# Optimization experiments

Hardware: AMD Instinct MI355X
Metric: run time of the kernel (lower is better)

The kernel has to match this reference:

```python
import jax, jax.numpy as jnp
import numpy as np
from jax import lax

EPS = 1e-7  # keras backend epsilon used by K.ctc_batch_cost
NEG = -1e30  # log-space 'zero'


def setup_inputs() -> dict:
    key = jax.random.key(0)
    k1, k2 = jax.random.split(key)
    B, T, C, L = 512, 512, 128, 48
    # softmax-like probabilities over classes (ctc_batch_cost expects probs)
    u = jax.random.uniform(k1, (B, T, C), dtype=jnp.float32, minval=1e-3, maxval=1.0)
    y_pred = u / jnp.sum(u, axis=-1, keepdims=True)
    # labels in [0, C-2]; blank index is C-1 (keras convention)
    y_true = jax.random.randint(k2, (B, L), 0, C - 1, dtype=jnp.int64)
    return {"y_true": y_true, "y_pred": y_pred}


def _ctc_loss(y_true, y_pred):
    # y_true: [B, L] int labels; y_pred: [B, T, C] probabilities
    B, T, C = y_pred.shape
    L = y_true.shape[1]
    S = 2 * L + 1
    blank = C - 1

    log_probs = jnp.log(y_pred + EPS)  # [B, T, C]

    # extended label sequence: blank, l1, blank, l2, ..., blank -> [B, S]
    ext = jnp.full((B, S), blank, dtype=y_true.dtype).at[:, 1::2].set(y_true)
    ext_m2 = jnp.concatenate(
        [jnp.full((B, 2), -1, dtype=ext.dtype), ext[:, :-2]], axis=1
    )
    # skip-transition allowed iff current symbol is a non-blank differing from s-2
    skip = (ext != blank) & (ext != ext_m2)  # [B, S]

    # gather per-extended-symbol log probs: [B, T, S] -> time-major [T, B, S]
    lp_ext = jnp.take_along_axis(log_probs, ext[:, None, :], axis=2)
    lp_ext = jnp.moveaxis(lp_ext, 1, 0)

    neg = jnp.asarray(NEG, log_probs.dtype)
    alpha0 = jnp.full((B, S), neg)
    alpha0 = alpha0.at[:, 0].set(lp_ext[0, :, 0]).at[:, 1].set(lp_ext[0, :, 1])

    def step(alpha, lp_t):
        a1 = alpha
        a2 = jnp.concatenate([jnp.full((B, 1), neg), alpha[:, :-1]], axis=1)
        a3 = jnp.concatenate([jnp.full((B, 2), neg), alpha[:, :-2]], axis=1)
        a3 = jnp.where(skip, a3, neg)
        new = jnp.logaddexp(jnp.logaddexp(a1, a2), a3) + lp_t
        return new, None

    alpha_T, _ = lax.scan(step, alpha0, lp_ext[1:])
    # total log-likelihood ends in last blank or last label
    loglik = jnp.logaddexp(alpha_T[:, -1], alpha_T[:, -2])
    return -loglik[:, None]  # [B, 1] like K.ctc_batch_cost


def reference(y_true, y_pred):
    return _ctc_loss(y_true, y_pred)
```

## Files before the change

kernel.cpp:

```cpp
#include <hip/hip_runtime.h>


constexpr int Bc = 512, Tc = 512, Cc = 128, Lc = 48;
constexpr double DEPS = 1e-7;
constexpr float FNEG = -1e30f;
constexpr float LN2F = 0.69314718055994530942f;

#define DPP_WAVE_SHR1 0x138
#define DPP_WAVE_SHL1 0x130

__device__ __forceinline__ double dpp64_shr1(double x) {
    long long u = __double_as_longlong(x);
    int a = __builtin_amdgcn_update_dpp(0, (int)u,         DPP_WAVE_SHR1, 0xF, 0xF, false);
    int b = __builtin_amdgcn_update_dpp(0, (int)(u >> 32), DPP_WAVE_SHR1, 0xF, 0xF, false);
    return __longlong_as_double(((long long)b << 32) | (unsigned int)a);
}
__device__ __forceinline__ double dpp64_shl1(double x) {
    long long u = __double_as_longlong(x);
    int a = __builtin_amdgcn_update_dpp(0, (int)u,         DPP_WAVE_SHL1, 0xF, 0xF, false);
    int b = __builtin_amdgcn_update_dpp(0, (int)(u >> 32), DPP_WAVE_SHL1, 0xF, 0xF, false);
    return __longlong_as_double(((long long)b << 32) | (unsigned int)a);
}

__device__ __forceinline__ float lae2(float a, float b) {
    float m = fmaxf(a, b);
    float d = fabsf(a - b);
    return m + __log2f(1.0f + __builtin_amdgcn_exp2f(-d));
}
__device__ __forceinline__ float blankpf(float praw) {
    return __uint_as_float((unsigned)
        __builtin_amdgcn_readlane(__float_as_uint(praw), 63));
}
__device__ __forceinline__ float log2d(double x) {
    if (!(x > 0.0)) return FNEG;
    long long u = __double_as_longlong(x);
    int e = (int)((u >> 52) & 0x7FF);
    if (e == 0) return FNEG;
    double m = __longlong_as_double((u & 0x000FFFFFFFFFFFFFLL) | 0x3FF0000000000000LL);
    return __log2f((float)m) + (float)(e - 1023);
}

__global__ __launch_bounds__(128)
void ctc_fb_kernel(const int* __restrict__ y_true,
                   const float* __restrict__ y_pred,
                   float* __restrict__ out) {
    const int b = blockIdx.x;
    const int lane = threadIdx.x & 63;
    const int wave = threadIdx.x >> 6;

    const float* yb = y_pred + (size_t)b * Tc * Cc;

    const int lab = (lane < Lc) ? y_true[b * Lc + lane] : (Cc - 1);
    const int labm1 = __builtin_amdgcn_ds_bpermute(((lane + 63) & 63) << 2, lab);
    const int labp1 = __builtin_amdgcn_ds_bpermute(((lane + 1) & 63) << 2, lab);
    const bool skip  = (lab != (Cc - 1)) && (lab != labm1);
    const bool skipN = (labp1 != (Cc - 1)) && (labp1 != lab);
    const bool validhi = (lane < Lc);
    const bool lane0 = (lane == 0);

    __shared__ double sblo[64], sbhi[64];
    __shared__ int sbc[64];

    double lo = 0.0, hi = 0.0;
    int c = 0;

    auto renorm = [&]() {
        double mx = fmax(lo, hi);
        #pragma unroll
        for (int mk = 1; mk < 64; mk <<= 1)
            mx = fmax(mx, __shfl_xor(mx, mk, 64));
        int e = (int)((__double_as_longlong(mx) >> 52) & 0x7FF) - 1023;
        double sc = __longlong_as_double((long long)(1023 - e) << 52);
        lo *= sc; hi *= sc;
        c += e;
    };

    if (wave == 0) {
        auto dostep = [&](float praw) {
            double pb = (double)blankpf(praw) + DEPS;
            double ph = validhi ? ((double)praw + DEPS) : 0.0;
            double sh = dpp64_shr1(hi);
            double a3 = skip ? sh : 0.0;
            double nlo = (lo + sh) * pb;
            double nhi = (hi + lo + a3) * ph;
            lo = nlo; hi = nhi;
        };
        float pf[32];
        #pragma unroll
        for (int j = 0; j < 32; ++j) pf[j] = yb[j * Cc + lab];
        {
            float praw = pf[0];
            pf[0] = yb[32 * Cc + lab];
            lo = lane0 ? ((double)blankpf(praw) + DEPS) : 0.0;
            hi = lane0 ? ((double)praw + DEPS) : 0.0;
            #pragma unroll
            for (int j = 1; j < 32; ++j) {
                float r = pf[j];
                pf[j] = yb[(32 + j) * Cc + lab];
                dostep(r);
            }
            renorm();
        }
        #pragma unroll 1
        for (int g = 1; g < 7; ++g) {
            const float* ybg = yb + (size_t)(g * 32 + 32) * Cc;
            #pragma unroll
            for (int j = 0; j < 32; ++j) {
                float r = pf[j];
                pf[j] = ybg[j * Cc + lab];
                dostep(r);
            }
            renorm();
        }
        #pragma unroll
        for (int j = 0; j < 32; ++j) dostep(pf[j]);
        renorm();
    } else {
        auto dostep = [&](float praw) {
            double pb = (double)blankpf(praw) + DEPS;
            double ph = validhi ? ((double)praw + DEPS) : 0.0;
            double qlo = lo * pb;
            double qhi = hi * ph;
            double qlo_n = dpp64_shl1(qlo);
            double qhi_n = dpp64_shl1(qhi);
            double nb = skipN ? (qlo_n + qhi_n) : qlo_n;
            lo = qlo + qhi;
            hi = qhi + nb;
        };
        lo = (lane == 48) ? 1.0 : 0.0;
        hi = (lane == 47) ? 1.0 : 0.0;
        float pf[32];
        #pragma unroll
        for (int j = 0; j < 32; ++j) pf[j] = yb[(size_t)(511 - j) * Cc + lab];
        #pragma unroll 1
        for (int g = 0; g < 7; ++g) {
            #pragma unroll
            for (int j = 0; j < 32; ++j) {
                float r = pf[j];
                pf[j] = yb[(size_t)(511 - (g * 32 + 32 + j)) * Cc + lab];
                dostep(r);
            }
            renorm();
        }
        #pragma unroll
        for (int j = 0; j < 32; ++j) dostep(pf[j]);
        renorm();
        sblo[lane] = lo;
        sbhi[lane] = hi;
        sbc[lane]  = c;
    }

    __syncthreads();

    if (wave == 0) {
        double plo = lo * sblo[lane];
        double phi = hi * sbhi[lane];
        float ctot = (float)(c + sbc[lane]);
        float yl = log2d(plo) + ctot;
        float yh = log2d(phi) + ctot;
        float v = lae2(yl, yh);
        #pragma unroll
        for (int mk = 1; mk < 64; mk <<= 1)
            v = lae2(v, __shfl_xor(v, mk, 64));
        if (lane0) out[b] = -(v * LN2F);
    }
}

extern "C" void kernel_launch(void* const* d_in, const int* in_sizes, int n_in,
                              void* d_out, int out_size, void* d_ws, size_t ws_size,
                              hipStream_t stream) {
    const int* y_true = (const int*)d_in[0];
    const float* y_pred = (const float*)d_in[1];
    float* out = (float*)d_out;
    hipLaunchKernelGGL(ctc_fb_kernel, dim3(Bc), dim3(128), 0, stream,
                       y_true, y_pred, out);
}
```

Before: 30.20 us.

## Stage probability rows into LDS with async global_load_lds double buffering

Per-lane strided register prefetches of label probabilities are replaced by full-row copies into a double-buffered LDS tile using global_load_lds. Each lane then gathers its label's value from LDS. The forward and backward waves now share one unified group loop, and epsilon is added in float. The aim is to hide global-load latency and make loads coalesced, at the cost of staging whole 128-class rows and relying on correct LDS-DMA wait handling, since only lgkmcnt is waited explicitly.

```diff
diff --git a/kernel.cpp b/kernel.cpp
--- a/kernel.cpp
+++ b/kernel.cpp
@@ -2,7 +2,7 @@
 
 
 constexpr int Bc = 512, Tc = 512, Cc = 128, Lc = 48;
-constexpr double DEPS = 1e-7;
+constexpr float FEPS = 1e-7f;
 constexpr float FNEG = -1e30f;
 constexpr float LN2F = 0.69314718055994530942f;
 
@@ -27,10 +27,6 @@
     float d = fabsf(a - b);
     return m + __log2f(1.0f + __builtin_amdgcn_exp2f(-d));
 }
-__device__ __forceinline__ float blankpf(float praw) {
-    return __uint_as_float((unsigned)
-        __builtin_amdgcn_readlane(__float_as_uint(praw), 63));
-}
 __device__ __forceinline__ float log2d(double x) {
     if (!(x > 0.0)) return FNEG;
     long long u = __double_as_longlong(x);
@@ -39,15 +35,27 @@
     double m = __longlong_as_double((u & 0x000FFFFFFFFFFFFFLL) | 0x3FF0000000000000LL);
     return __log2f((float)m) + (float)(e - 1023);
 }
+__device__ __forceinline__ float rdlane63(float v) {
+    return __uint_as_float((unsigned)__builtin_amdgcn_readlane(__float_as_uint(v), 63));
+}
+
+typedef const __attribute__((address_space(1))) void* gptr_t;
+typedef __attribute__((address_space(3))) void* lptr_t;
+__device__ __forceinline__ void gload(const float* g, float* l) {
+    __builtin_amdgcn_global_load_lds((gptr_t)g, (lptr_t)l, 4, 0, 0);
+}
 
 __global__ __launch_bounds__(128)
 void ctc_fb_kernel(const int* __restrict__ y_true,
                    const float* __restrict__ y_pred,
                    float* __restrict__ out) {
+    __shared__ float rowbuf[2][2][32][Cc];
+    __shared__ double sblo[64], sbhi[64];
+    __shared__ int sbc[64];
+
     const int b = blockIdx.x;
     const int lane = threadIdx.x & 63;
     const int wave = threadIdx.x >> 6;
-
     const float* yb = y_pred + (size_t)b * Tc * Cc;
 
     const int lab = (lane < Lc) ? y_true[b * Lc + lane] : (Cc - 1);
@@ -55,11 +63,22 @@
     const int labp1 = __builtin_amdgcn_ds_bpermute(((lane + 1) & 63) << 2, lab);
     const bool skip  = (lab != (Cc - 1)) && (lab != labm1);
     const bool skipN = (labp1 != (Cc - 1)) && (labp1 != lab);
-    const bool validhi = (lane < Lc);
     const bool lane0 = (lane == 0);
 
-    __shared__ double sblo[64], sbhi[64];
-    __shared__ int sbc[64];
+    float (*buf)[32][Cc] = rowbuf[wave];
+    const ptrdiff_t rs = wave ? -(ptrdiff_t)Cc : (ptrdiff_t)Cc;
+    const float* g0 = yb + (wave ? (size_t)(Tc - 1) * Cc : 0) + lane;
+
+    auto stage = [&](int pg, int g) {
+        const float* gb = g0 + (ptrdiff_t)(g * 32) * rs;
+        float* lb = &buf[pg][0][0];
+        #pragma unroll
+        for (int j = 0; j < 32; ++j) {
+            const float* gr = gb + (ptrdiff_t)j * rs;
+            gload(gr, lb + j * Cc);
+            gload(gr + 64, lb + j * Cc + 64);
+        }
+    };
 
     double lo = 0.0, hi = 0.0;
     int c = 0;
@@ -75,86 +94,81 @@
         c += e;
     };
 
+    float praw[32];
+    auto readgrp = [&](int pg) {
+        #pragma unroll
+        for (int j = 0; j < 32; ++j) praw[j] = buf[pg][j][lab];
+        asm volatile("s_waitcnt lgkmcnt(0)" ::: "memory");
+    };
+
+    auto fstep = [&](float pr) {
+        float pe = pr + FEPS;
+        double ph = (double)pe;
+        double pb = (double)rdlane63(pe);
+        double sh = dpp64_shr1(hi);
+        double a3 = skip ? sh : 0.0;
+        double nlo = (lo + sh) * pb;
+        double nhi = (hi + lo + a3) * ph;
+        lo = nlo; hi = nhi;
+    };
+    auto bstep = [&](float pr) {
+        float pe = (lane == 48) ? 0.0f : pr + FEPS;
+        double ph = (double)pe;
+        double pb = (double)rdlane63(pr + FEPS);
+        double qlo = lo * pb;
+        double qhi = hi * ph;
+        double qlo_n = dpp64_shl1(qlo);
+        double qhi_n = dpp64_shl1(qhi);
+        double nb = skipN ? (qlo_n + qhi_n) : qlo_n;
+        lo = qlo + qhi;
+        hi = qhi + nb;
+    };
+
+    stage(0, 0);
+    stage(1, 1);
+
+    readgrp(0);
+    stage(0, 2);
     if (wave == 0) {
-        auto dostep = [&](float praw) {
-            double pb = (double)blankpf(praw) + DEPS;
-            double ph = validhi ? ((double)praw + DEPS) : 0.0;
-            double sh = dpp64_shr1(hi);
-            double a3 = skip ? sh : 0.0;
-            double nlo = (lo + sh) * pb;
-            double nhi = (hi + lo + a3) * ph;
-            lo = nlo; hi = nhi;
-        };
-        float pf[32];
+        float pe = praw[0] + FEPS;
+        float pbf = rdlane63(pe);
+        lo = lane0 ? (double)pbf : 0.0;
+        hi = lane0 ? (double)pe : 0.0;
         #pragma unroll
-        for (int j = 0; j < 32; ++j) pf[j] = yb[j * Cc + lab];
-        {
-            float praw = pf[0];
-            pf[0] = yb[32 * Cc + lab];
-            lo = lane0 ? ((double)blankpf(praw) + DEPS) : 0.0;
-            hi = lane0 ? ((double)praw + DEPS) : 0.0;
-            #pragma unroll
-            for (int j = 1; j < 32; ++j) {
-                float r = pf[j];
-                pf[j] = yb[(32 + j) * Cc + lab];
-                dostep(r);
-            }
-            renorm();
-        }
-        #pragma unroll 1
-        for (int g = 1; g < 7; ++g) {
-            const float* ybg = yb + (size_t)(g * 32 + 32) * Cc;
-            #pragma unroll
-            for (int j = 0; j < 32; ++j) {
-                float r = pf[j];
-                pf[j] = ybg[j * Cc + lab];
-                dostep(r);
-            }
-            renorm();
-        }
-        #pragma unroll
-        for (int j = 0; j < 32; ++j) dostep(pf[j]);
-        renorm();
+        for (int j = 1; j < 32; ++j) fstep(praw[j]);
     } else {
-        auto dostep = [&](float praw) {
-            double pb = (double)blankpf(praw) + DEPS;
-            double ph = validhi ? ((double)praw + DEPS) : 0.0;
-            double qlo = lo * pb;
-            double qhi = hi * ph;
-            double qlo_n = dpp64_shl1(qlo);
-            double qhi_n = dpp64_shl1(qhi);
-            double nb = skipN ? (qlo_n + qhi_n) : qlo_n;
-            lo = qlo + qhi;
-            hi = qhi + nb;
-        };
         lo = (lane == 48) ? 1.0 : 0.0;
         hi = (lane == 47) ? 1.0 : 0.0;
-        float pf[32];
         #pragma unroll
-        for (int j = 0; j < 32; ++j) pf[j] = yb[(size_t)(511 - j) * Cc + lab];
-        #pragma unroll 1
-        for (int g = 0; g < 7; ++g) {
+        for (int j = 0; j < 32; ++j) bstep(praw[j]);
+    }
+    renorm();
+
+    #pragma unroll 1
+    for (int g = 1; g < 8; ++g) {
+        const int pg = g & 1;
+        readgrp(pg);
+        if (g < 6) stage(pg, g + 2);
+        if (wave == 0) {
             #pragma unroll
-            for (int j = 0; j < 32; ++j) {
-                float r = pf[j];
-                pf[j] = yb[(size_t)(511 - (g * 32 + 32 + j)) * Cc + lab];
-                dostep(r);
-            }
-            renorm();
+            for (int j = 0; j < 32; ++j) fstep(praw[j]);
+        } else {
+            #pragma unroll
+            for (int j = 0; j < 32; ++j) bstep(praw[j]);
         }
-        #pragma unroll
-        for (int j = 0; j < 32; ++j) dostep(pf[j]);
         renorm();
+    }
+
+    if (wave == 1) {
         sblo[lane] = lo;
         sbhi[lane] = hi;
         sbc[lane]  = c;
     }
-
     __syncthreads();
 
     if (wave == 0) {
-        double plo = lo * sblo[lane];
-        double phi = hi * sbhi[lane];
+        double plo = (lane <= 48) ? lo * sblo[lane] : 0.0;
+        double phi = (lane <= 47) ? hi * sbhi[lane] : 0.0;
         float ctot = (float)(c + sbc[lane]);
         float yl = log2d(plo) + ctot;
         float yh = log2d(phi) + ctot;
```

After: 31.38 us. 1.04x slower.

## Batch probability conversion, reformulate backward step with one DPP shift, cheaper renorm

Applied to the files above, without the earlier changes.

Restructures the forward and backward recursions to precompute blank and label probabilities (readlane, double conversion, epsilon add) in batches of 16 ahead of the serial dependency chain, with the next batch's loads issued before the steps. The backward step is reformulated so the skip term uses the current lane's skip flag and only one 64-bit DPP shift is needed per step instead of two. Renormalization now reduces integer exponents instead of doubles and runs every 32 steps. This shortens the latency-bound critical path but adds register pressure from the 16-entry double arrays, and exposes load latency at batch boundaries.

```diff
diff --git a/kernel.cpp b/kernel.cpp
--- a/kernel.cpp
+++ b/kernel.cpp
@@ -27,9 +27,9 @@
     float d = fabsf(a - b);
     return m + __log2f(1.0f + __builtin_amdgcn_exp2f(-d));
 }
-__device__ __forceinline__ float blankpf(float praw) {
+__device__ __forceinline__ float rd63f(float v) {
     return __uint_as_float((unsigned)
-        __builtin_amdgcn_readlane(__float_as_uint(praw), 63));
+        __builtin_amdgcn_readlane(__float_as_uint(v), 63));
 }
 __device__ __forceinline__ float log2d(double x) {
     if (!(x > 0.0)) return FNEG;
@@ -52,9 +52,7 @@
 
     const int lab = (lane < Lc) ? y_true[b * Lc + lane] : (Cc - 1);
     const int labm1 = __builtin_amdgcn_ds_bpermute(((lane + 63) & 63) << 2, lab);
-    const int labp1 = __builtin_amdgcn_ds_bpermute(((lane + 1) & 63) << 2, lab);
     const bool skip  = (lab != (Cc - 1)) && (lab != labm1);
-    const bool skipN = (labp1 != (Cc - 1)) && (labp1 != lab);
     const bool validhi = (lane < Lc);
     const bool lane0 = (lane == 0);
 
@@ -66,85 +64,85 @@
 
     auto renorm = [&]() {
         double mx = fmax(lo, hi);
+        int eb = (int)((__double_as_longlong(mx) >> 52) & 0x7FF);
         #pragma unroll
         for (int mk = 1; mk < 64; mk <<= 1)
-            mx = fmax(mx, __shfl_xor(mx, mk, 64));
-        int e = (int)((__double_as_longlong(mx) >> 52) & 0x7FF) - 1023;
+            eb = max(eb, __shfl_xor(eb, mk, 64));
+        int e = eb - 1023;
         double sc = __longlong_as_double((long long)(1023 - e) << 52);
         lo *= sc; hi *= sc;
         c += e;
     };
 
+    float praw[16];
+    double pb64[16], ph64[16];
+
+    auto batch = [&]() {
+        #pragma unroll
+        for (int j = 0; j < 16; ++j) {
+            pb64[j] = (double)rd63f(praw[j]) + DEPS;
+            ph64[j] = validhi ? ((double)praw[j] + DEPS) : 0.0;
+        }
+    };
+
     if (wave == 0) {
-        auto dostep = [&](float praw) {
-            double pb = (double)blankpf(praw) + DEPS;
-            double ph = validhi ? ((double)praw + DEPS) : 0.0;
+        auto step = [&](int j) {
             double sh = dpp64_shr1(hi);
             double a3 = skip ? sh : 0.0;
-            double nlo = (lo + sh) * pb;
-            double nhi = (hi + lo + a3) * ph;
+            double nlo = (lo + sh) * pb64[j];
+            double nhi = ((hi + lo) + a3) * ph64[j];
             lo = nlo; hi = nhi;
         };
-        float pf[32];
         #pragma unroll
-        for (int j = 0; j < 32; ++j) pf[j] = yb[j * Cc + lab];
+        for (int j = 0; j < 16; ++j) praw[j] = yb[j * Cc + lab];
         {
-            float praw = pf[0];
-            pf[0] = yb[32 * Cc + lab];
-            lo = lane0 ? ((double)blankpf(praw) + DEPS) : 0.0;
-            hi = lane0 ? ((double)praw + DEPS) : 0.0;
+            batch();
+            const float* ybn = yb + (size_t)16 * Cc + lab;
             #pragma unroll
-            for (int j = 1; j < 32; ++j) {
-                float r = pf[j];
-                pf[j] = yb[(32 + j) * Cc + lab];
-                dostep(r);
-            }
-            renorm();
+            for (int j = 0; j < 16; ++j) praw[j] = ybn[(size_t)j * Cc];
+            lo = lane0 ? pb64[0] : 0.0;
+            hi = lane0 ? ph64[0] : 0.0;
+            #pragma unroll
+            for (int j = 1; j < 16; ++j) step(j);
         }
         #pragma unroll 1
-        for (int g = 1; g < 7; ++g) {
-            const float* ybg = yb + (size_t)(g * 32 + 32) * Cc;
+        for (int g = 1; g < 16; ++g) {
+            batch();
+            if (g < 15) {
+                const float* ybn = yb + (size_t)((g + 1) * 16) * Cc + lab;
+                #pragma unroll
+                for (int j = 0; j < 16; ++j) praw[j] = ybn[(size_t)j * Cc];
+            }
             #pragma unroll
-            for (int j = 0; j < 32; ++j) {
-                float r = pf[j];
-                pf[j] = ybg[j * Cc + lab];
-                dostep(r);
-            }
-            renorm();
+            for (int j = 0; j < 16; ++j) step(j);
+            if (g & 1) renorm();
         }
-        #pragma unroll
-        for (int j = 0; j < 32; ++j) dostep(pf[j]);
-        renorm();
     } else {
-        auto dostep = [&](float praw) {
-            double pb = (double)blankpf(praw) + DEPS;
-            double ph = validhi ? ((double)praw + DEPS) : 0.0;
-            double qlo = lo * pb;
-            double qhi = hi * ph;
-            double qlo_n = dpp64_shl1(qlo);
-            double qhi_n = dpp64_shl1(qhi);
-            double nb = skipN ? (qlo_n + qhi_n) : qlo_n;
+        auto step = [&](int j) {
+            double qlo = lo * pb64[j];
+            double qhi = hi * ph64[j];
+            double u  = qlo + (skip ? qhi : 0.0);
+            double nb = dpp64_shl1(u);
             lo = qlo + qhi;
             hi = qhi + nb;
         };
         lo = (lane == 48) ? 1.0 : 0.0;
         hi = (lane == 47) ? 1.0 : 0.0;
-        float pf[32];
         #pragma unroll
-        for (int j = 0; j < 32; ++j) pf[j] = yb[(size_t)(511 - j) * Cc + lab];
+        for (int j = 0; j < 16; ++j) praw[j] = yb[(size_t)(511 - j) * Cc + lab];
         #pragma unroll 1
-        for (int g = 0; g < 7; ++g) {
+        for (int g = 0; g < 16; ++g) {
+            batch();
+            if (g < 15) {
+                const float* ybn = yb + lab;
+                const int t0 = 511 - (g + 1) * 16;
+                #pragma unroll
+                for (int j = 0; j < 16; ++j) praw[j] = ybn[(size_t)(t0 - j) * Cc];
+            }
             #pragma unroll
-            for (int j = 0; j < 32; ++j) {
-                float r = pf[j];
-                pf[j] = yb[(size_t)(511 - (g * 32 + 32 + j)) * Cc + lab];
-                dostep(r);
-            }
-            renorm();
+            for (int j = 0; j < 16; ++j) step(j);
+            if (g & 1) renorm();
         }
-        #pragma unroll
-        for (int j = 0; j < 32; ++j) dostep(pf[j]);
-        renorm();
         sblo[lane] = lo;
         sbhi[lane] = hi;
         sbc[lane]  = c;
```

Result: faster. 28.99 us, median of 2 (-4.0%).
